# Performance work log

Measured on AMD Instinct MI355X. Metric: run time of the kernel, lower is better.

## Reference

```python
import jax, jax.numpy as jnp
import numpy as np

B, C, D = 2048, 1000, 256


def setup_inputs() -> dict:
    key = jax.random.key(0)
    k1, k2 = jax.random.split(key)
    x = jax.random.normal(k1, (B, D), dtype=jnp.float32)
    # xavier_uniform for prototypes [C, D]: bound = sqrt(6 / (C + D))
    bound = np.sqrt(6.0 / (C + D)).astype(np.float32)
    prototypes = jax.random.uniform(k2, (C, D), dtype=jnp.float32,
                                    minval=-bound, maxval=bound)
    log_diag = jnp.zeros((C, D), dtype=jnp.float32)
    return {"x": x, "prototypes": prototypes, "log_diag": log_diag}


def reference(x, prototypes, log_diag):
    # diff: [B, C, D] broadcast of x against class prototypes
    diff = x[:, None, :] - prototypes[None, :, :]
    precision_diag = jnp.exp(log_diag)  # [C, D]
    # per-class diagonal-weighted squared distance, reduced over features
    mahalanobis_sq = jnp.sum(diff * diff * precision_diag[None, :, :], axis=2)  # [B, C]
    return -mahalanobis_sq
```

## Files before the change

### kernel.cpp

```cpp
#include <hip/hip_runtime.h>


#define C_N 1000
#define D_N 256

typedef __attribute__((ext_vector_type(8))) short bf16x8;
typedef __attribute__((ext_vector_type(4))) float f32x4;

__device__ inline short f2bf(float f) {
  unsigned int u = __float_as_uint(f);
  unsigned int lsb = (u >> 16) & 1u;
  u += 0x7fffu + lsb;
  return (short)(u >> 16);
}

__device__ inline bf16x8 pack8(const float* v) {
  bf16x8 o;
#pragma unroll
  for (int j = 0; j < 8; ++j) o[j] = f2bf(v[j]);
  return o;
}

__global__ __launch_bounds__(256, 2) void mahal_fused(
    const float* __restrict__ x, const float* __restrict__ p,
    const float* __restrict__ ld, float* __restrict__ out) {
  __shared__ short lA[4][8][64][8];
  __shared__ short lB[4][8][64][8];
  __shared__ float s_lds[64];

  const int tid = threadIdx.x;
  const int w   = tid >> 6;
  const int l   = tid & 63;
  const int r16 = l & 15;
  const int hi  = l >> 4;
  const int bx  = blockIdx.x;
  const int by  = blockIdx.y;

  bf16x8 xa_sv[8];
  bf16x8 pw_sv[8];

  {
    const int c = by * 64 + w * 16 + r16;
    const bool valid = (c < C_N);
    float sp = 0.f;
#pragma unroll
    for (int t = 0; t < 8; ++t) {
      const int d = t * 32 + hi * 8;
      float wv[8], pwv[8];
      if (valid) {
        const float* lp = ld + (size_t)c * D_N + d;
        const float* pp = p  + (size_t)c * D_N + d;
        float4 l0 = *reinterpret_cast<const float4*>(lp);
        float4 l1 = *reinterpret_cast<const float4*>(lp + 4);
        float4 p0 = *reinterpret_cast<const float4*>(pp);
        float4 p1 = *reinterpret_cast<const float4*>(pp + 4);
        float lv[8] = {l0.x,l0.y,l0.z,l0.w,l1.x,l1.y,l1.z,l1.w};
        float pv[8] = {p0.x,p0.y,p0.z,p0.w,p1.x,p1.y,p1.z,p1.w};
#pragma unroll
        for (int j = 0; j < 8; ++j) {
          float wj = __expf(lv[j]);
          wv[j]  = wj;
          pwv[j] = -2.f * pv[j] * wj;
          sp += pv[j] * pv[j] * wj;
        }
      } else {
#pragma unroll
        for (int j = 0; j < 8; ++j) { wv[j] = 0.f; pwv[j] = 0.f; }
      }
      *reinterpret_cast<bf16x8*>(&lB[w][t][l][0]) = pack8(wv);
      pw_sv[t] = pack8(pwv);
    }
    sp += __shfl_xor(sp, 16, 64);
    sp += __shfl_xor(sp, 32, 64);
    if (l < 16) s_lds[w * 16 + r16] = sp;

    const int row = bx * 64 + w * 16 + r16;
#pragma unroll
    for (int t = 0; t < 8; ++t) {
      const int d = t * 32 + hi * 8;
      const float* xp = x + (size_t)row * D_N + d;
      float4 v0 = *reinterpret_cast<const float4*>(xp);
      float4 v1 = *reinterpret_cast<const float4*>(xp + 4);
      float v[8] = {v0.x,v0.y,v0.z,v0.w,v1.x,v1.y,v1.z,v1.w};
      float sq[8];
#pragma unroll
      for (int j = 0; j < 8; ++j) sq[j] = v[j] * v[j];
      *reinterpret_cast<bf16x8*>(&lA[w][t][l][0]) = pack8(sq);
      xa_sv[t] = pack8(v);
    }
  }
  __syncthreads();

  const int wm = w >> 1, wn = w & 1;
  f32x4 acc[2][2];
#pragma unroll
  for (int i = 0; i < 2; ++i)
#pragma unroll
    for (int jn = 0; jn < 2; ++jn) acc[i][jn] = {0.f, 0.f, 0.f, 0.f};

#pragma unroll
  for (int kt = 0; kt < 8; ++kt) {
    bf16x8 a0 = *reinterpret_cast<const bf16x8*>(&lA[wm * 2 + 0][kt][l][0]);
    bf16x8 a1 = *reinterpret_cast<const bf16x8*>(&lA[wm * 2 + 1][kt][l][0]);
    bf16x8 b0 = *reinterpret_cast<const bf16x8*>(&lB[wn * 2 + 0][kt][l][0]);
    bf16x8 b1 = *reinterpret_cast<const bf16x8*>(&lB[wn * 2 + 1][kt][l][0]);
    acc[0][0] = __builtin_amdgcn_mfma_f32_16x16x32_bf16(a0, b0, acc[0][0], 0, 0, 0);
    acc[0][1] = __builtin_amdgcn_mfma_f32_16x16x32_bf16(a0, b1, acc[0][1], 0, 0, 0);
    acc[1][0] = __builtin_amdgcn_mfma_f32_16x16x32_bf16(a1, b0, acc[1][0], 0, 0, 0);
    acc[1][1] = __builtin_amdgcn_mfma_f32_16x16x32_bf16(a1, b1, acc[1][1], 0, 0, 0);
  }
  __syncthreads();

#pragma unroll
  for (int t = 0; t < 8; ++t) {
    *reinterpret_cast<bf16x8*>(&lA[w][t][l][0]) = xa_sv[t];
    *reinterpret_cast<bf16x8*>(&lB[w][t][l][0]) = pw_sv[t];
  }
  __syncthreads();

#pragma unroll
  for (int kt = 0; kt < 8; ++kt) {
    bf16x8 a0 = *reinterpret_cast<const bf16x8*>(&lA[wm * 2 + 0][kt][l][0]);
    bf16x8 a1 = *reinterpret_cast<const bf16x8*>(&lA[wm * 2 + 1][kt][l][0]);
    bf16x8 b0 = *reinterpret_cast<const bf16x8*>(&lB[wn * 2 + 0][kt][l][0]);
    bf16x8 b1 = *reinterpret_cast<const bf16x8*>(&lB[wn * 2 + 1][kt][l][0]);
    acc[0][0] = __builtin_amdgcn_mfma_f32_16x16x32_bf16(a0, b0, acc[0][0], 0, 0, 0);
    acc[0][1] = __builtin_amdgcn_mfma_f32_16x16x32_bf16(a0, b1, acc[0][1], 0, 0, 0);
    acc[1][0] = __builtin_amdgcn_mfma_f32_16x16x32_bf16(a1, b0, acc[1][0], 0, 0, 0);
    acc[1][1] = __builtin_amdgcn_mfma_f32_16x16x32_bf16(a1, b1, acc[1][1], 0, 0, 0);
  }

  const int colbase = by * 64 + wn * 32 + r16;
  const int rowbase = bx * 64 + wm * 32 + hi * 4;
#pragma unroll
  for (int jn = 0; jn < 2; ++jn) {
    const int col = colbase + jn * 16;
    if (col < C_N) {
      const float sc = s_lds[wn * 32 + jn * 16 + r16];
#pragma unroll
      for (int i = 0; i < 2; ++i) {
        const int row = rowbase + i * 16;
#pragma unroll
        for (int r = 0; r < 4; ++r)
          out[(size_t)(row + r) * C_N + col] = -(acc[i][jn][r] + sc);
      }
    }
  }
}

extern "C" void kernel_launch(void* const* d_in, const int* in_sizes, int n_in,
                              void* d_out, int out_size, void* d_ws, size_t ws_size,
                              hipStream_t stream) {
  const float* x  = (const float*)d_in[0];
  const float* p  = (const float*)d_in[1];
  const float* ld = (const float*)d_in[2];
  float* out = (float*)d_out;
  mahal_fused<<<dim3(32, 16), 256, 0, stream>>>(x, p, ld, out);
}
```

Before: 20.08 us.

## Double block row tile to 128 with 512 threads and split prototype prep

Each block now covers 128 batch rows instead of 64 with 8 waves. The prototype/log_diag preprocessing is split across two wave halves by feature dimension, and both the weight and scaled-prototype bf16 tiles are kept in LDS, so the per-class exp work is done half as many times overall. It also swaps the manual bf16 rounding for the packed __float22bfloat162_rn intrinsic. The grid halves to 256 blocks, which may reduce occupancy or parallelism across CUs.

```diff
diff --git a/kernel.cpp b/kernel.cpp
--- a/kernel.cpp
+++ b/kernel.cpp
@@ -1,4 +1,5 @@
 #include <hip/hip_runtime.h>
+#include <hip/hip_bf16.h>
 
 
 #define C_N 1000
@@ -7,26 +8,20 @@
 typedef __attribute__((ext_vector_type(8))) short bf16x8;
 typedef __attribute__((ext_vector_type(4))) float f32x4;
 
-__device__ inline short f2bf(float f) {
-  unsigned int u = __float_as_uint(f);
-  unsigned int lsb = (u >> 16) & 1u;
-  u += 0x7fffu + lsb;
-  return (short)(u >> 16);
+__device__ inline bf16x8 pack8(const float* v) {
+  union { bf16x8 o; __hip_bfloat162 h[4]; } u;
+#pragma unroll
+  for (int j = 0; j < 4; ++j)
+    u.h[j] = __float22bfloat162_rn(make_float2(v[2 * j], v[2 * j + 1]));
+  return u.o;
 }
 
-__device__ inline bf16x8 pack8(const float* v) {
-  bf16x8 o;
-#pragma unroll
-  for (int j = 0; j < 8; ++j) o[j] = f2bf(v[j]);
-  return o;
-}
-
-__global__ __launch_bounds__(256, 2) void mahal_fused(
+__global__ __launch_bounds__(512, 2) void mahal_fused(
     const float* __restrict__ x, const float* __restrict__ p,
     const float* __restrict__ ld, float* __restrict__ out) {
-  __shared__ short lA[4][8][64][8];
-  __shared__ short lB[4][8][64][8];
-  __shared__ float s_lds[64];
+  __shared__ short lA[8][8][64][8];
+  __shared__ short lB[4][16][64][8];
+  __shared__ float s_lds[2][64];
 
   const int tid = threadIdx.x;
   const int w   = tid >> 6;
@@ -37,15 +32,16 @@
   const int by  = blockIdx.y;
 
   bf16x8 xa_sv[8];
-  bf16x8 pw_sv[8];
 
   {
-    const int c = by * 64 + w * 16 + r16;
+    const int ct = w & 3;
+    const int dh = w >> 2;
+    const int c  = by * 64 + ct * 16 + r16;
     const bool valid = (c < C_N);
     float sp = 0.f;
 #pragma unroll
-    for (int t = 0; t < 8; ++t) {
-      const int d = t * 32 + hi * 8;
+    for (int t = 0; t < 4; ++t) {
+      const int d = dh * 128 + t * 32 + hi * 8;
       float wv[8], pwv[8];
       if (valid) {
         const float* lp = ld + (size_t)c * D_N + d;
@@ -67,14 +63,16 @@
 #pragma unroll
         for (int j = 0; j < 8; ++j) { wv[j] = 0.f; pwv[j] = 0.f; }
       }
-      *reinterpret_cast<bf16x8*>(&lB[w][t][l][0]) = pack8(wv);
-      pw_sv[t] = pack8(pwv);
+      *reinterpret_cast<bf16x8*>(&lB[ct][dh * 4 + t][l][0])     = pack8(wv);
+      *reinterpret_cast<bf16x8*>(&lB[ct][8 + dh * 4 + t][l][0]) = pack8(pwv);
     }
     sp += __shfl_xor(sp, 16, 64);
     sp += __shfl_xor(sp, 32, 64);
-    if (l < 16) s_lds[w * 16 + r16] = sp;
+    if (l < 16) s_lds[dh][ct * 16 + r16] = sp;
+  }
 
-    const int row = bx * 64 + w * 16 + r16;
+  {
+    const int row = bx * 128 + w * 16 + r16;
 #pragma unroll
     for (int t = 0; t < 8; ++t) {
       const int d = t * 32 + hi * 8;
@@ -112,18 +110,16 @@
   __syncthreads();
 
 #pragma unroll
-  for (int t = 0; t < 8; ++t) {
+  for (int t = 0; t < 8; ++t)
     *reinterpret_cast<bf16x8*>(&lA[w][t][l][0]) = xa_sv[t];
-    *reinterpret_cast<bf16x8*>(&lB[w][t][l][0]) = pw_sv[t];
-  }
   __syncthreads();
 
 #pragma unroll
   for (int kt = 0; kt < 8; ++kt) {
     bf16x8 a0 = *reinterpret_cast<const bf16x8*>(&lA[wm * 2 + 0][kt][l][0]);
     bf16x8 a1 = *reinterpret_cast<const bf16x8*>(&lA[wm * 2 + 1][kt][l][0]);
-    bf16x8 b0 = *reinterpret_cast<const bf16x8*>(&lB[wn * 2 + 0][kt][l][0]);
-    bf16x8 b1 = *reinterpret_cast<const bf16x8*>(&lB[wn * 2 + 1][kt][l][0]);
+    bf16x8 b0 = *reinterpret_cast<const bf16x8*>(&lB[wn * 2 + 0][8 + kt][l][0]);
+    bf16x8 b1 = *reinterpret_cast<const bf16x8*>(&lB[wn * 2 + 1][8 + kt][l][0]);
     acc[0][0] = __builtin_amdgcn_mfma_f32_16x16x32_bf16(a0, b0, acc[0][0], 0, 0, 0);
     acc[0][1] = __builtin_amdgcn_mfma_f32_16x16x32_bf16(a0, b1, acc[0][1], 0, 0, 0);
     acc[1][0] = __builtin_amdgcn_mfma_f32_16x16x32_bf16(a1, b0, acc[1][0], 0, 0, 0);
@@ -131,12 +127,13 @@
   }
 
   const int colbase = by * 64 + wn * 32 + r16;
-  const int rowbase = bx * 64 + wm * 32 + hi * 4;
+  const int rowbase = bx * 128 + wm * 32 + hi * 4;
 #pragma unroll
   for (int jn = 0; jn < 2; ++jn) {
     const int col = colbase + jn * 16;
     if (col < C_N) {
-      const float sc = s_lds[wn * 32 + jn * 16 + r16];
+      const int ci = wn * 32 + jn * 16 + r16;
+      const float sc = s_lds[0][ci] + s_lds[1][ci];
 #pragma unroll
       for (int i = 0; i < 2; ++i) {
         const int row = rowbase + i * 16;
@@ -155,5 +152,5 @@
   const float* p  = (const float*)d_in[1];
   const float* ld = (const float*)d_in[2];
   float* out = (float*)d_out;
-  mahal_fused<<<dim3(32, 16), 256, 0, stream>>>(x, p, ld, out);
+  mahal_fused<<<dim3(16, 16), 512, 0, stream>>>(x, p, ld, out);
 }
```

Result: faster. 17.04 us (-15.1%).
